# Optimization experiments

Measured on AMD Instinct MI355X. Metric: run time of the kernel, lower is better.

The kernel has to match this reference:

```python
import jax, jax.numpy as jnp
import numpy as np

# --- geometry constants (ProtoDUNE-HD-like) ---
B, F, T = 1, 1, 256            # batch, input features, nticks
NCHANS = 2560                   # total readout channels (800+800+480+480)
NWIRES = [800, 800, 480]        # wires per plane (U, V, W) on each face
NCELLS = 40000                  # number of 3-wire crossing cells per face
MLP_HID, MLP_OUT = 8, 2

# channel ranges per (face, plane): induction planes (U,V) wrap both faces,
# collection (W) channels are disjoint per face
_CHAN_RANGES = {(0, 0): (0, 800), (0, 1): (800, 1600), (0, 2): (1600, 2080),
                (1, 0): (0, 800), (1, 1): (800, 1600), (1, 2): (2080, 2560)}


def _make_tables():
    rng = np.random.default_rng(0)
    wcs = {}
    for (f, p), (lo, hi) in _CHAN_RANGES.items():
        n = hi - lo
        ch = lo + rng.permutation(n)                       # irregular wire->channel map
        wcs[(f, p)] = np.stack([np.arange(n), ch], axis=1).astype(np.int64)
    gi = {}
    for f in (0, 1):
        gi[f] = np.stack([rng.integers(0, NWIRES[p], NCELLS) for p in range(3)],
                         axis=1).astype(np.int64)          # (NCELLS, 3) wire idx per plane
    return wcs, gi


def setup_inputs() -> dict:
    key = jax.random.key(0)
    k = jax.random.split(key, 5)
    wcs, gi = _make_tables()
    inp = {
        'x':  jax.random.normal(k[0], (B, F, NCHANS, T), jnp.float32),
        'W1': jax.random.normal(k[1], (3 * F, MLP_HID), jnp.float32) * 0.5,
        'b1': jax.random.normal(k[2], (MLP_HID,), jnp.float32) * 0.1,
        'W2': jax.random.normal(k[3], (MLP_HID, MLP_OUT), jnp.float32) * 0.5,
        'b2': jax.random.normal(k[4], (MLP_OUT,), jnp.float32) * 0.1,
        'gi0': jnp.asarray(gi[0]), 'gi1': jnp.asarray(gi[1]),
    }
    for f in (0, 1):
        for p in range(3):
            inp[f'wc{f}{p}'] = jnp.asarray(wcs[(f, p)])
    return inp


def _make_wires(x, wc):
    # wires[..., wire_ident, :] = x[..., channel, :]   (Network.make_wires)
    Bb, Ff, _, Tt = x.shape
    wires = jnp.zeros((Bb, Ff, wc.shape[0], Tt), x.dtype)
    return wires.at[:, :, wc[:, 0], :].set(x[:, :, wc[:, 1], :])


def _crossview_mlp(x, W1, b1, W2, b2, wcs, gis):
    # mp_step: relu -> per-face cross-view gather -> MLP -> amax scatter -> concat
    x = jax.nn.relu(x)
    Bb, Ff, C, Tt = x.shape
    scattered = jnp.zeros((Bb, MLP_OUT, C, Tt), x.dtype)   # zeros init => amax includes 0
    for f in range(2):
        gi = gis[f]
        # gather the three plane views for each crossing cell: (B, 3F, NCELLS, T)
        cells = jnp.concatenate(
            [_make_wires(x, wcs[f][p])[:, :, gi[:, p], :] for p in range(3)], axis=1)
        h = jnp.einsum('bfnt,fh->bhnt', cells, W1) + b1[None, :, None, None]
        y = jnp.einsum('bhnt,ho->bont', h, W2) + b2[None, :, None, None]
        # scatter_to_chans: amax-reduce cell outputs back onto readout channels
        for p in range(3):
            ch = wcs[f][p][gi[:, p], 1]                    # channel of each cell's wire
            scattered = scattered.at[:, :, ch, :].max(y)
    # special_style == 'mlp': concat input features with cross-view MLP features
    return jnp.concatenate([x, scattered], axis=1)         # (B, F+MLP_OUT, C, T)


def reference(x, W1, b1, W2, b2, wc00, wc01, wc02, wc10, wc11, wc12, gi0, gi1):
    wcs = ((wc00, wc01, wc02), (wc10, wc11, wc12))
    gis = (gi0, gi1)
    return _crossview_mlp(x, W1, b1, W2, b2, wcs, gis)
```

## Files before the change

kernel.cpp:

```cpp
#include <hip/hip_runtime.h>
#include <hip/hip_fp16.h>

#define NCHANS 2560
#define TT 256
#define NINST 240000
#define HALF_NINST 120000
#define CAP 192

#define WS_CURSOR 0
#define WS_XR     16384
#define WS_EPACK  1327104

#define PREP_BLOCKS 640
#define FILL_BLOCKS 938

__device__ __forceinline__ __half2 pk_max_f16(__half2 a, __half2 b) {
    unsigned int ua = *(unsigned int*)&a;
    unsigned int ub = *(unsigned int*)&b;
    unsigned int ur;
    asm("v_pk_max_f16 %0, %1, %2" : "=v"(ur) : "v"(ua), "v"(ub));
    return *(__half2*)&ur;
}
__device__ __forceinline__ __half2 u2h(unsigned int u) { return *(__half2*)&u; }
__device__ __forceinline__ unsigned int h2u(__half2 h) { return *(unsigned int*)&h; }

__global__ __launch_bounds__(256) void zero_cursor_kernel(int* __restrict__ cursor) {
    cursor[blockIdx.x * 256 + threadIdx.x] = 0;
}

__global__ __launch_bounds__(256) void prep_fill_kernel(
    const float* __restrict__ x,
    const int* __restrict__ gi0, const int* __restrict__ gi1,
    const int* __restrict__ wc00, const int* __restrict__ wc01, const int* __restrict__ wc02,
    const int* __restrict__ wc10, const int* __restrict__ wc11, const int* __restrict__ wc12,
    int* __restrict__ cursor, unsigned int* __restrict__ epack, uint2* __restrict__ xr,
    float* __restrict__ out)
{
    const int b = blockIdx.x;
    if (b < PREP_BLOCKS) {
        const int i = b * 256 + threadIdx.x;
        float4 v = ((const float4*)x)[i];
        v.x = fmaxf(v.x, 0.f); v.y = fmaxf(v.y, 0.f);
        v.z = fmaxf(v.z, 0.f); v.w = fmaxf(v.w, 0.f);
        ((float4*)out)[i] = v;
        __half2 h01 = __floats2half2_rn(v.x, v.y);
        __half2 h23 = __floats2half2_rn(v.z, v.w);
        uint2 p;
        p.x = h2u(h01);
        p.y = h2u(h23);
        xr[i] = p;
    } else {
        const int j = (b - PREP_BLOCKS) * 256 + threadIdx.x;
        if (j >= NINST) return;
        const int face = (j >= HALF_NINST) ? 1 : 0;
        const int i = j - face * HALF_NINST;
        const int p = i % 3;
        const int cellBase = i - p;
        const int* gi = face ? gi1 : gi0;
        const int w0 = gi[cellBase + 0];
        const int w1 = gi[cellBase + 1];
        const int w2 = gi[cellBase + 2];
        const int* wcA = face ? wc10 : wc00;
        const int* wcB = face ? wc11 : wc01;
        const int* wcC = face ? wc12 : wc02;
        const int c0 = wcA[w0 * 2 + 1];
        const int c1 = wcB[w1 * 2 + 1];
        const int c2 = wcC[w2 * 2 + 1];
        const int cOwn = (p == 0) ? c0 : ((p == 1) ? c1 : c2);
        const int cA   = (p == 0) ? c1 : c0;
        const int cB   = (p == 2) ? c1 : c2;
        const unsigned int E = (unsigned)cA | ((unsigned)cB << 16);
        const int s = atomicAdd(&cursor[cOwn], 1);
        if (s < CAP) epack[cOwn * CAP + s] = E;
    }
}

__global__ __launch_bounds__(256, 8) void gather_kernel(
    const float* __restrict__ W1, const float* __restrict__ b1,
    const float* __restrict__ W2, const float* __restrict__ b2,
    const int* __restrict__ cursor, const unsigned int* __restrict__ epack,
    const uint2* __restrict__ xr, float* __restrict__ out)
{
    float Af[3][2], Cf[2];
#pragma unroll
    for (int o = 0; o < 2; ++o) {
        float s = b2[o];
#pragma unroll
        for (int h = 0; h < 8; ++h) s += b1[h] * W2[h * 2 + o];
        Cf[o] = s;
    }
#pragma unroll
    for (int p = 0; p < 3; ++p)
#pragma unroll
        for (int o = 0; o < 2; ++o) {
            float s = 0.f;
#pragma unroll
            for (int h = 0; h < 8; ++h) s += W1[p * 8 + h] * W2[h * 2 + o];
            Af[p][o] = s;
        }
    __half2 a2[3][2], C2[2];
#pragma unroll
    for (int p = 0; p < 3; ++p)
#pragma unroll
        for (int o = 0; o < 2; ++o) a2[p][o] = __half2half2(__float2half(Af[p][o]));
    C2[0] = __half2half2(__float2half(Cf[0]));
    C2[1] = __half2half2(__float2half(Cf[1]));

    __shared__ unsigned int sEnt[CAP];
    __shared__ uint4 sM[3][64];

    const int w = threadIdx.x >> 6;
    const int lane = threadIdx.x & 63;
    const int ch = __builtin_amdgcn_readfirstlane(blockIdx.x);

    int n = cursor[ch];
    n = n < CAP ? n : CAP;

    if ((int)threadIdx.x < n) sEnt[threadIdx.x] = epack[ch * CAP + threadIdx.x];
    __syncthreads();

    const int p = (ch >= 1600) ? 2 : ((ch >= 800) ? 1 : 0);
    const int pA = (p == 0) ? 1 : 0;
    const int pB = (p == 2) ? 1 : 2;
    const __half2 aA0 = a2[pA][0], aB0 = a2[pB][0];
    const __half2 aA1 = a2[pA][1], aB1 = a2[pB][1];

    const uint2 dOwn = xr[ch * 64 + lane];
    const __half2 base00 = __hfma2(a2[p][0], u2h(dOwn.x), C2[0]);
    const __half2 base01 = __hfma2(a2[p][0], u2h(dOwn.y), C2[0]);
    const __half2 base10 = __hfma2(a2[p][1], u2h(dOwn.x), C2[1]);
    const __half2 base11 = __hfma2(a2[p][1], u2h(dOwn.y), C2[1]);

    const int lo = (n * w) >> 2;
    const int hi = (n * (w + 1)) >> 2;

    __half2 m00 = __half2half2(__float2half(0.f));
    __half2 m01 = m00, m10 = m00, m11 = m00;

#pragma unroll 4
    for (int e = lo; e < hi; ++e) {
        const unsigned int E = sEnt[e];
        const int cA = E & 0xFFFFu;
        const int cB = E >> 16;
        const uint2 dA = xr[cA * 64 + lane];
        const uint2 dB = xr[cB * 64 + lane];
        const __half2 y00 = __hfma2(aA0, u2h(dA.x), __hfma2(aB0, u2h(dB.x), base00));
        const __half2 y01 = __hfma2(aA0, u2h(dA.y), __hfma2(aB0, u2h(dB.y), base01));
        const __half2 y10 = __hfma2(aA1, u2h(dA.x), __hfma2(aB1, u2h(dB.x), base10));
        const __half2 y11 = __hfma2(aA1, u2h(dA.y), __hfma2(aB1, u2h(dB.y), base11));
        m00 = pk_max_f16(m00, y00); m01 = pk_max_f16(m01, y01);
        m10 = pk_max_f16(m10, y10); m11 = pk_max_f16(m11, y11);
    }

    if (w) sM[w - 1][lane] = make_uint4(h2u(m00), h2u(m01), h2u(m10), h2u(m11));
    __syncthreads();
    if (w == 0) {
#pragma unroll
        for (int q = 0; q < 3; ++q) {
            const uint4 o = sM[q][lane];
            m00 = pk_max_f16(m00, u2h(o.x));
            m01 = pk_max_f16(m01, u2h(o.y));
            m10 = pk_max_f16(m10, u2h(o.z));
            m11 = pk_max_f16(m11, u2h(o.w));
        }
        const int off = ch * TT + lane * 4;
        *(float4*)(out + NCHANS * TT + off) =
            make_float4(__low2float(m00), __high2float(m00), __low2float(m01), __high2float(m01));
        *(float4*)(out + 2 * NCHANS * TT + off) =
            make_float4(__low2float(m10), __high2float(m10), __low2float(m11), __high2float(m11));
    }
}

extern "C" void kernel_launch(void* const* d_in, const int* in_sizes, int n_in,
                              void* d_out, int out_size, void* d_ws, size_t ws_size,
                              hipStream_t stream) {
    const float* x  = (const float*)d_in[0];
    const float* W1 = (const float*)d_in[1];
    const float* b1 = (const float*)d_in[2];
    const float* W2 = (const float*)d_in[3];
    const float* b2 = (const float*)d_in[4];
    const int* gi0  = (const int*)d_in[5];
    const int* gi1  = (const int*)d_in[6];
    const int* wc00 = (const int*)d_in[7];
    const int* wc01 = (const int*)d_in[8];
    const int* wc02 = (const int*)d_in[9];
    const int* wc10 = (const int*)d_in[10];
    const int* wc11 = (const int*)d_in[11];
    const int* wc12 = (const int*)d_in[12];
    float* out = (float*)d_out;

    char* ws = (char*)d_ws;
    int*          cursor = (int*)(ws + WS_CURSOR);
    uint2*        xr     = (uint2*)(ws + WS_XR);
    unsigned int* epack  = (unsigned int*)(ws + WS_EPACK);

    zero_cursor_kernel<<<NCHANS / 256, 256, 0, stream>>>(cursor);

    prep_fill_kernel<<<PREP_BLOCKS + FILL_BLOCKS, 256, 0, stream>>>(
        x, gi0, gi1, wc00, wc01, wc02, wc10, wc11, wc12,
        cursor, epack, xr, out);

    gather_kernel<<<NCHANS, 256, 0, stream>>>(
        W1, b1, W2, b2, cursor, epack, xr, out);
}
```

Measured before the change: 79.58 us.

## Split gather per channel into two T-halves and stage neighbor rows via direct global-to-LDS loads

Each channel is now handled by two blocks, each covering half of the time axis. Each block first issues global_load_lds direct-to-LDS copies of every neighbor row it needs, waits once on all of them, then runs the FMA/max loop from LDS. The aim is to put all gather loads in flight at once instead of serialising them through registers, and to double the block count for better latency hiding. The cost is a large LDS buffer (about 78 KB) that limits occupancy. CAP is also lowered to 152, which silently truncates any channel with more entries.

```diff
diff --git a/kernel.cpp b/kernel.cpp
--- a/kernel.cpp
+++ b/kernel.cpp
@@ -5,7 +5,7 @@
 #define TT 256
 #define NINST 240000
 #define HALF_NINST 120000
-#define CAP 192
+#define CAP 152
 
 #define WS_CURSOR 0
 #define WS_XR     16384
@@ -13,6 +13,9 @@
 
 #define PREP_BLOCKS 640
 #define FILL_BLOCKS 938
+
+typedef const unsigned int __attribute__((address_space(1)))* glb_u32p;
+typedef unsigned int __attribute__((address_space(3)))* lds_u32p;
 
 __device__ __forceinline__ __half2 pk_max_f16(__half2 a, __half2 b) {
     unsigned int ua = *(unsigned int*)&a;
@@ -75,7 +78,7 @@
     }
 }
 
-__global__ __launch_bounds__(256, 8) void gather_kernel(
+__global__ __launch_bounds__(256, 2) void gather_kernel(
     const float* __restrict__ W1, const float* __restrict__ b1,
     const float* __restrict__ W2, const float* __restrict__ b2,
     const int* __restrict__ cursor, const unsigned int* __restrict__ epack,
@@ -107,11 +110,13 @@
     C2[1] = __half2half2(__float2half(Cf[1]));
 
     __shared__ unsigned int sEnt[CAP];
-    __shared__ uint4 sM[3][64];
+    __shared__ unsigned int rows[CAP * 128];
+    __shared__ uint2 sM[3][64];
 
     const int w = threadIdx.x >> 6;
     const int lane = threadIdx.x & 63;
-    const int ch = __builtin_amdgcn_readfirstlane(blockIdx.x);
+    const int ch = __builtin_amdgcn_readfirstlane((int)blockIdx.x >> 1);
+    const int half = blockIdx.x & 1;
 
     int n = cursor[ch];
     n = n < CAP ? n : CAP;
@@ -125,49 +130,50 @@
     const __half2 aA0 = a2[pA][0], aB0 = a2[pB][0];
     const __half2 aA1 = a2[pA][1], aB1 = a2[pB][1];
 
-    const uint2 dOwn = xr[ch * 64 + lane];
-    const __half2 base00 = __hfma2(a2[p][0], u2h(dOwn.x), C2[0]);
-    const __half2 base01 = __hfma2(a2[p][0], u2h(dOwn.y), C2[0]);
-    const __half2 base10 = __hfma2(a2[p][1], u2h(dOwn.x), C2[1]);
-    const __half2 base11 = __hfma2(a2[p][1], u2h(dOwn.y), C2[1]);
+    const unsigned int* xru = (const unsigned int*)xr;
+    const int lane_off = half * 64 + lane;
+
+    const unsigned int dOwn = xru[ch * 128 + lane_off];
+    const __half2 base0 = __hfma2(a2[p][0], u2h(dOwn), C2[0]);
+    const __half2 base1 = __hfma2(a2[p][1], u2h(dOwn), C2[1]);
 
     const int lo = (n * w) >> 2;
     const int hi = (n * (w + 1)) >> 2;
 
-    __half2 m00 = __half2half2(__float2half(0.f));
-    __half2 m01 = m00, m10 = m00, m11 = m00;
-
+    for (int e = lo; e < hi; ++e) {
+        const unsigned int E = sEnt[e];
+        const unsigned int* ga = xru + (E & 0xFFFFu) * 128 + lane_off;
+        const unsigned int* gb = xru + (E >> 16) * 128 + lane_off;
+        __builtin_amdgcn_global_load_lds((glb_u32p)ga, (lds_u32p)&rows[e * 128], 4, 0, 0);
+        __builtin_amdgcn_global_load_lds((glb_u32p)gb, (lds_u32p)&rows[e * 128 + 64], 4, 0, 0);
+    }
+    asm volatile("s_waitcnt vmcnt(0)" ::: "memory");
+    __builtin_amdgcn_sched_barrier(0);
+
+    __half2 m0 = __half2half2(__float2half(0.f));
+    __half2 m1 = m0;
 #pragma unroll 4
     for (int e = lo; e < hi; ++e) {
-        const unsigned int E = sEnt[e];
-        const int cA = E & 0xFFFFu;
-        const int cB = E >> 16;
-        const uint2 dA = xr[cA * 64 + lane];
-        const uint2 dB = xr[cB * 64 + lane];
-        const __half2 y00 = __hfma2(aA0, u2h(dA.x), __hfma2(aB0, u2h(dB.x), base00));
-        const __half2 y01 = __hfma2(aA0, u2h(dA.y), __hfma2(aB0, u2h(dB.y), base01));
-        const __half2 y10 = __hfma2(aA1, u2h(dA.x), __hfma2(aB1, u2h(dB.x), base10));
-        const __half2 y11 = __hfma2(aA1, u2h(dA.y), __hfma2(aB1, u2h(dB.y), base11));
-        m00 = pk_max_f16(m00, y00); m01 = pk_max_f16(m01, y01);
-        m10 = pk_max_f16(m10, y10); m11 = pk_max_f16(m11, y11);
-    }
-
-    if (w) sM[w - 1][lane] = make_uint4(h2u(m00), h2u(m01), h2u(m10), h2u(m11));
+        const unsigned int a = rows[e * 128 + lane];
+        const unsigned int b = rows[e * 128 + 64 + lane];
+        const __half2 y0 = __hfma2(aA0, u2h(a), __hfma2(aB0, u2h(b), base0));
+        const __half2 y1 = __hfma2(aA1, u2h(a), __hfma2(aB1, u2h(b), base1));
+        m0 = pk_max_f16(m0, y0);
+        m1 = pk_max_f16(m1, y1);
+    }
+
+    if (w) sM[w - 1][lane] = make_uint2(h2u(m0), h2u(m1));
     __syncthreads();
     if (w == 0) {
 #pragma unroll
         for (int q = 0; q < 3; ++q) {
-            const uint4 o = sM[q][lane];
-            m00 = pk_max_f16(m00, u2h(o.x));
-            m01 = pk_max_f16(m01, u2h(o.y));
-            m10 = pk_max_f16(m10, u2h(o.z));
-            m11 = pk_max_f16(m11, u2h(o.w));
+            const uint2 o = sM[q][lane];
+            m0 = pk_max_f16(m0, u2h(o.x));
+            m1 = pk_max_f16(m1, u2h(o.y));
         }
-        const int off = ch * TT + lane * 4;
-        *(float4*)(out + NCHANS * TT + off) =
-            make_float4(__low2float(m00), __high2float(m00), __low2float(m01), __high2float(m01));
-        *(float4*)(out + 2 * NCHANS * TT + off) =
-            make_float4(__low2float(m10), __high2float(m10), __low2float(m11), __high2float(m11));
+        const int off = ch * TT + half * 128 + lane * 2;
+        *(float2*)(out + NCHANS * TT + off)     = make_float2(__low2float(m0), __high2float(m0));
+        *(float2*)(out + 2 * NCHANS * TT + off) = make_float2(__low2float(m1), __high2float(m1));
     }
 }
 
@@ -200,6 +206,6 @@
         x, gi0, gi1, wc00, wc01, wc02, wc10, wc11, wc12,
         cursor, epack, xr, out);
 
-    gather_kernel<<<NCHANS, 256, 0, stream>>>(
+    gather_kernel<<<NCHANS * 2, 256, 0, stream>>>(
         W1, b1, W2, b2, cursor, epack, xr, out);
 }
```

Measured after the change: 92.57 us. +16.3%, slower.

## Tile time axis so each block stages all channels' slice in LDS for gathers

Applied to the files above, without the earlier changes.

The relu'd half-precision input is stored tile-major, 32 time tiles of 8 samples across all 2560 channels, so one gather block can copy a 40KB tile into shared memory. Each block then serves 128 channels for that tile, doing the cross-view gathers from LDS instead of scattered global loads. Two threads split each channel's entry list and merge through shared memory. CAP drops from 192 to 152, which risks silently truncating cells if a channel has more entries. The kernel also loses its occupancy hint, and the epack list is now read from global memory per thread instead of being staged.

```diff
diff --git a/kernel.cpp b/kernel.cpp
--- a/kernel.cpp
+++ b/kernel.cpp
@@ -5,10 +5,13 @@
 #define TT 256
 #define NINST 240000
 #define HALF_NINST 120000
-#define CAP 192
+#define CAP 152
+#define NTILE 32
+#define NGRP 20
+#define GRP_CH 128
 
 #define WS_CURSOR 0
-#define WS_XR     16384
+#define WS_XRT    16384
 #define WS_EPACK  1327104
 
 #define PREP_BLOCKS 640
@@ -33,7 +36,7 @@
     const int* __restrict__ gi0, const int* __restrict__ gi1,
     const int* __restrict__ wc00, const int* __restrict__ wc01, const int* __restrict__ wc02,
     const int* __restrict__ wc10, const int* __restrict__ wc11, const int* __restrict__ wc12,
-    int* __restrict__ cursor, unsigned int* __restrict__ epack, uint2* __restrict__ xr,
+    int* __restrict__ cursor, unsigned int* __restrict__ epack, unsigned int* __restrict__ xrt,
     float* __restrict__ out)
 {
     const int b = blockIdx.x;
@@ -45,10 +48,13 @@
         ((float4*)out)[i] = v;
         __half2 h01 = __floats2half2_rn(v.x, v.y);
         __half2 h23 = __floats2half2_rn(v.z, v.w);
-        uint2 p;
-        p.x = h2u(h01);
-        p.y = h2u(h23);
-        xr[i] = p;
+        const int ch = i >> 6;
+        const int q = i & 63;
+        const int tile = q >> 1;
+        const int slot = (q & 1) << 1;
+        unsigned int* dst = xrt + ((tile * NCHANS + ch) << 2) + slot;
+        dst[0] = h2u(h01);
+        dst[1] = h2u(h23);
     } else {
         const int j = (b - PREP_BLOCKS) * 256 + threadIdx.x;
         if (j >= NINST) return;
@@ -75,12 +81,27 @@
     }
 }
 
-__global__ __launch_bounds__(256, 8) void gather_kernel(
+__global__ __launch_bounds__(256) void gather_kernel(
     const float* __restrict__ W1, const float* __restrict__ b1,
     const float* __restrict__ W2, const float* __restrict__ b2,
     const int* __restrict__ cursor, const unsigned int* __restrict__ epack,
-    const uint2* __restrict__ xr, float* __restrict__ out)
+    const unsigned int* __restrict__ xrt, float* __restrict__ out)
 {
+    __shared__ unsigned int sTile[NCHANS * 4];
+    __shared__ unsigned int sPart[128][8];
+
+    const int tid = threadIdx.x;
+    const int tile = blockIdx.x / NGRP;
+    const int grp  = blockIdx.x % NGRP;
+
+    {
+        const uint4* src4 = (const uint4*)(xrt + tile * NCHANS * 4);
+        uint4* dst4 = (uint4*)sTile;
+#pragma unroll
+        for (int k = 0; k < 10; ++k) dst4[k * 256 + tid] = src4[k * 256 + tid];
+    }
+    __syncthreads();
+
     float Af[3][2], Cf[2];
 #pragma unroll
     for (int o = 0; o < 2; ++o) {
@@ -106,68 +127,74 @@
     C2[0] = __half2half2(__float2half(Cf[0]));
     C2[1] = __half2half2(__float2half(Cf[1]));
 
-    __shared__ unsigned int sEnt[CAP];
-    __shared__ uint4 sM[3][64];
-
-    const int w = threadIdx.x >> 6;
-    const int lane = threadIdx.x & 63;
-    const int ch = __builtin_amdgcn_readfirstlane(blockIdx.x);
-
-    int n = cursor[ch];
-    n = n < CAP ? n : CAP;
-
-    if ((int)threadIdx.x < n) sEnt[threadIdx.x] = epack[ch * CAP + threadIdx.x];
-    __syncthreads();
-
-    const int p = (ch >= 1600) ? 2 : ((ch >= 800) ? 1 : 0);
+    const int c = grp * GRP_CH + (tid & 127);
+    const int half = tid >> 7;
+
+    const int p = (c >= 1600) ? 2 : ((c >= 800) ? 1 : 0);
     const int pA = (p == 0) ? 1 : 0;
     const int pB = (p == 2) ? 1 : 2;
     const __half2 aA0 = a2[pA][0], aB0 = a2[pB][0];
     const __half2 aA1 = a2[pA][1], aB1 = a2[pB][1];
 
-    const uint2 dOwn = xr[ch * 64 + lane];
-    const __half2 base00 = __hfma2(a2[p][0], u2h(dOwn.x), C2[0]);
-    const __half2 base01 = __hfma2(a2[p][0], u2h(dOwn.y), C2[0]);
-    const __half2 base10 = __hfma2(a2[p][1], u2h(dOwn.x), C2[1]);
-    const __half2 base11 = __hfma2(a2[p][1], u2h(dOwn.y), C2[1]);
-
-    const int lo = (n * w) >> 2;
-    const int hi = (n * (w + 1)) >> 2;
+    const uint4 own = *(const uint4*)&sTile[c << 2];
+    const __half2 b00 = __hfma2(a2[p][0], u2h(own.x), C2[0]);
+    const __half2 b01 = __hfma2(a2[p][0], u2h(own.y), C2[0]);
+    const __half2 b02 = __hfma2(a2[p][0], u2h(own.z), C2[0]);
+    const __half2 b03 = __hfma2(a2[p][0], u2h(own.w), C2[0]);
+    const __half2 b10 = __hfma2(a2[p][1], u2h(own.x), C2[1]);
+    const __half2 b11 = __hfma2(a2[p][1], u2h(own.y), C2[1]);
+    const __half2 b12 = __hfma2(a2[p][1], u2h(own.z), C2[1]);
+    const __half2 b13 = __hfma2(a2[p][1], u2h(own.w), C2[1]);
+
+    int n = cursor[c];
+    n = n < CAP ? n : CAP;
+    const int n2 = n >> 1;
+    const int lo = half ? n2 : 0;
+    const int hi = half ? n : n2;
+    const unsigned int* ep = epack + c * CAP;
 
     __half2 m00 = __half2half2(__float2half(0.f));
-    __half2 m01 = m00, m10 = m00, m11 = m00;
-
-#pragma unroll 4
+    __half2 m01 = m00, m02 = m00, m03 = m00;
+    __half2 m10 = m00, m11 = m00, m12 = m00, m13 = m00;
+
     for (int e = lo; e < hi; ++e) {
-        const unsigned int E = sEnt[e];
-        const int cA = E & 0xFFFFu;
-        const int cB = E >> 16;
-        const uint2 dA = xr[cA * 64 + lane];
-        const uint2 dB = xr[cB * 64 + lane];
-        const __half2 y00 = __hfma2(aA0, u2h(dA.x), __hfma2(aB0, u2h(dB.x), base00));
-        const __half2 y01 = __hfma2(aA0, u2h(dA.y), __hfma2(aB0, u2h(dB.y), base01));
-        const __half2 y10 = __hfma2(aA1, u2h(dA.x), __hfma2(aB1, u2h(dB.x), base10));
-        const __half2 y11 = __hfma2(aA1, u2h(dA.y), __hfma2(aB1, u2h(dB.y), base11));
-        m00 = pk_max_f16(m00, y00); m01 = pk_max_f16(m01, y01);
-        m10 = pk_max_f16(m10, y10); m11 = pk_max_f16(m11, y11);
-    }
-
-    if (w) sM[w - 1][lane] = make_uint4(h2u(m00), h2u(m01), h2u(m10), h2u(m11));
+        const unsigned int E = ep[e];
+        const uint4 A = *(const uint4*)&sTile[(E & 0xFFFFu) << 2];
+        const uint4 B = *(const uint4*)&sTile[(E >> 16) << 2];
+        m00 = pk_max_f16(m00, __hfma2(aA0, u2h(A.x), __hfma2(aB0, u2h(B.x), b00)));
+        m01 = pk_max_f16(m01, __hfma2(aA0, u2h(A.y), __hfma2(aB0, u2h(B.y), b01)));
+        m02 = pk_max_f16(m02, __hfma2(aA0, u2h(A.z), __hfma2(aB0, u2h(B.z), b02)));
+        m03 = pk_max_f16(m03, __hfma2(aA0, u2h(A.w), __hfma2(aB0, u2h(B.w), b03)));
+        m10 = pk_max_f16(m10, __hfma2(aA1, u2h(A.x), __hfma2(aB1, u2h(B.x), b10)));
+        m11 = pk_max_f16(m11, __hfma2(aA1, u2h(A.y), __hfma2(aB1, u2h(B.y), b11)));
+        m12 = pk_max_f16(m12, __hfma2(aA1, u2h(A.z), __hfma2(aB1, u2h(B.z), b12)));
+        m13 = pk_max_f16(m13, __hfma2(aA1, u2h(A.w), __hfma2(aB1, u2h(B.w), b13)));
+    }
+
+    if (half) {
+        unsigned int* d = sPart[tid - 128];
+        d[0] = h2u(m00); d[1] = h2u(m01); d[2] = h2u(m02); d[3] = h2u(m03);
+        d[4] = h2u(m10); d[5] = h2u(m11); d[6] = h2u(m12); d[7] = h2u(m13);
+    }
     __syncthreads();
-    if (w == 0) {
-#pragma unroll
-        for (int q = 0; q < 3; ++q) {
-            const uint4 o = sM[q][lane];
-            m00 = pk_max_f16(m00, u2h(o.x));
-            m01 = pk_max_f16(m01, u2h(o.y));
-            m10 = pk_max_f16(m10, u2h(o.z));
-            m11 = pk_max_f16(m11, u2h(o.w));
-        }
-        const int off = ch * TT + lane * 4;
-        *(float4*)(out + NCHANS * TT + off) =
-            make_float4(__low2float(m00), __high2float(m00), __low2float(m01), __high2float(m01));
-        *(float4*)(out + 2 * NCHANS * TT + off) =
-            make_float4(__low2float(m10), __high2float(m10), __low2float(m11), __high2float(m11));
+    if (!half) {
+        const unsigned int* s = sPart[tid];
+        m00 = pk_max_f16(m00, u2h(s[0])); m01 = pk_max_f16(m01, u2h(s[1]));
+        m02 = pk_max_f16(m02, u2h(s[2])); m03 = pk_max_f16(m03, u2h(s[3]));
+        m10 = pk_max_f16(m10, u2h(s[4])); m11 = pk_max_f16(m11, u2h(s[5]));
+        m12 = pk_max_f16(m12, u2h(s[6])); m13 = pk_max_f16(m13, u2h(s[7]));
+
+        const int off = c * TT + tile * 8;
+        float* o1 = out + NCHANS * TT + off;
+        float* o2 = out + 2 * NCHANS * TT + off;
+        *(float4*)(o1)     = make_float4(__low2float(m00), __high2float(m00),
+                                         __low2float(m01), __high2float(m01));
+        *(float4*)(o1 + 4) = make_float4(__low2float(m02), __high2float(m02),
+                                         __low2float(m03), __high2float(m03));
+        *(float4*)(o2)     = make_float4(__low2float(m10), __high2float(m10),
+                                         __low2float(m11), __high2float(m11));
+        *(float4*)(o2 + 4) = make_float4(__low2float(m12), __high2float(m12),
+                                         __low2float(m13), __high2float(m13));
     }
 }
 
@@ -191,15 +218,15 @@
 
     char* ws = (char*)d_ws;
     int*          cursor = (int*)(ws + WS_CURSOR);
-    uint2*        xr     = (uint2*)(ws + WS_XR);
+    unsigned int* xrt    = (unsigned int*)(ws + WS_XRT);
     unsigned int* epack  = (unsigned int*)(ws + WS_EPACK);
 
     zero_cursor_kernel<<<NCHANS / 256, 256, 0, stream>>>(cursor);
 
     prep_fill_kernel<<<PREP_BLOCKS + FILL_BLOCKS, 256, 0, stream>>>(
         x, gi0, gi1, wc00, wc01, wc02, wc10, wc11, wc12,
-        cursor, epack, xr, out);
-
-    gather_kernel<<<NCHANS, 256, 0, stream>>>(
-        W1, b1, W2, b2, cursor, epack, xr, out);
-}
+        cursor, epack, xrt, out);
+
+    gather_kernel<<<NTILE * NGRP, 256, 0, stream>>>(
+        W1, b1, W2, b2, cursor, epack, xrt, out);
+}
```

New measurement: 104.3 us. 1.31x slower.
